# Kernel optimization log

Measured on AMD Instinct MI355X. Metric: run time of the kernel, lower is better.

Reference implementation:

```python
import jax, jax.numpy as jnp
import numpy as np

N = 50000       # nodes
E = 1600000     # edges (avg degree 32)
F_IN = 128      # input node features
HID = 64        # hidden_dim
H = 2           # heads in conv1
NEG_SLOPE = 0.2 # PyG GATConv default


def gat_conv(x, W, a_src, a_dst, b, src, dst, heads, out_ch):
    """PyG-style GATConv (concat=True). x:[n,f], W:[f,heads*out_ch],
    a_src/a_dst:[heads,out_ch], b:[heads*out_ch], src/dst:[e]."""
    n = x.shape[0]
    xh = (x @ W).reshape(n, heads, out_ch)              # [n,H,C]
    s_src = jnp.sum(xh * a_src[None], axis=-1)          # [n,H]
    s_dst = jnp.sum(xh * a_dst[None], axis=-1)          # [n,H]
    e = jax.nn.leaky_relu(s_src[src] + s_dst[dst], NEG_SLOPE)  # [e,H]
    # segment softmax over incoming edges of each destination node
    emax = jax.ops.segment_max(e, dst, num_segments=n)  # [n,H]
    emax = jnp.where(jnp.isfinite(emax), emax, 0.0)
    p = jnp.exp(e - emax[dst])
    denom = jax.ops.segment_sum(p, dst, num_segments=n)
    alpha = p / (denom[dst] + 1e-16)                    # [e,H]
    out = jax.ops.segment_sum(xh[src] * alpha[..., None], dst, num_segments=n)
    return out.reshape(n, heads * out_ch) + b


def setup_inputs() -> dict:
    key = jax.random.key(0)
    ks = jax.random.split(key, 14)
    g = lambda k, shape, fan: jax.random.normal(k, shape, jnp.float32) / np.sqrt(fan).astype(np.float32)
    return {
        "x": jax.random.normal(ks[0], (N, F_IN), jnp.float32),
        "edge_index": jax.random.randint(ks[1], (2, E), 0, N, jnp.int32),
        "W1": g(ks[2], (F_IN, H * HID), F_IN),
        "a_src1": g(ks[3], (H, HID), HID),
        "a_dst1": g(ks[4], (H, HID), HID),
        "b1": jnp.zeros((H * HID,), jnp.float32),
        "W2": g(ks[5], (H * HID, HID), H * HID),
        "a_src2": g(ks[6], (1, HID), HID),
        "a_dst2": g(ks[7], (1, HID), HID),
        "b2": jnp.zeros((HID,), jnp.float32),
        "Wm": g(ks[8], (HID, 1), HID),
        "bm": jnp.zeros((1,), jnp.float32),
        "Wl": g(ks[9], (HID, 4), HID),
        "bl": jnp.zeros((4,), jnp.float32),
    }


def reference(x, edge_index, W1, a_src1, a_dst1, b1, W2, a_src2, a_dst2, b2, Wm, bm, Wl, bl):
    n = x.shape[0]
    loop = jnp.arange(n, dtype=edge_index.dtype)        # PyG add_self_loops=True
    src = jnp.concatenate([edge_index[0], loop])
    dst = jnp.concatenate([edge_index[1], loop])
    h = jax.nn.relu(gat_conv(x, W1, a_src1, a_dst1, b1, src, dst, H, HID))
    # dropout layers are identity in eval mode
    h = jax.nn.relu(gat_conv(h, W2, a_src2, a_dst2, b2, src, dst, 1, HID))
    mortality = h @ Wm + bm   # [n,1]
    los = h @ Wl + bl         # [n,4]
    return (mortality, los)
```

## Files before the change

kernel.cpp:

```cpp
#include <hip/hip_runtime.h>
#include <hip/hip_bf16.h>

typedef __hip_bfloat16 bf16;
typedef __attribute__((ext_vector_type(8))) short short8;
typedef __attribute__((ext_vector_type(4))) float f32x4;

static __device__ __forceinline__ float b2f(const bf16 v){ return __bfloat162float(v); }
static __device__ __forceinline__ float lrelu(float x){ return x > 0.f ? x : 0.2f * x; }

static __device__ __forceinline__ float ldf(const void* p, size_t i, int f32){
  return f32 ? ((const float*)p)[i] : __bfloat162float(((const bf16*)p)[i]);
}

static __device__ __forceinline__ float wsum(float v){
#pragma unroll
  for (int o = 32; o; o >>= 1) v += __shfl_xor(v, o, 64);
  return v;
}
static __device__ __forceinline__ float wmax(float v){
#pragma unroll
  for (int o = 32; o; o >>= 1) v = fmaxf(v, __shfl_xor(v, o, 64));
  return v;
}
static __device__ __forceinline__ float qsum(float v){
  v += __shfl_xor(v, 1); v += __shfl_xor(v, 2);
  v += __shfl_xor(v, 4); v += __shfl_xor(v, 8);
  return v;
}

static __device__ __forceinline__ unsigned short f2bf(float x){
  unsigned u = __float_as_uint(x);
  unsigned r = (u + 0x7fffu + ((u >> 16) & 1u)) >> 16;
  return (unsigned short)r;
}
static __device__ __forceinline__ float bfval(unsigned short h){
  return __uint_as_float(((unsigned)h) << 16);
}
static __device__ __forceinline__ unsigned packbf2(float a, float b){
  return ((unsigned)f2bf(b) << 16) | (unsigned)f2bf(a);
}
static __device__ __forceinline__ float unlo(unsigned v){ return __uint_as_float(v << 16); }
static __device__ __forceinline__ float unhi(unsigned v){ return __uint_as_float(v & 0xffff0000u); }

__global__ void k_detect(const unsigned short* __restrict__ x, int* __restrict__ flag,
                         int* __restrict__ bucketCur, int nbuck){
  __shared__ int cnt;
  if (threadIdx.x == 0) cnt = 0;
  __syncthreads();
  int bad = 0;
  for (int i = threadIdx.x; i < 8192; i += 256){
    int e = (x[i] >> 7) & 0xFF;
    if (e >= 133) bad++;
  }
  atomicAdd(&cnt, bad);
  for (int i = threadIdx.x; i < nbuck; i += 256) bucketCur[i] = 0;
  __syncthreads();
  if (threadIdx.x == 0) *flag = (cnt > 16) ? 1 : 0;
}

#define CAP 10240
#define EPB 16
#define CHUNK (256 * EPB)

__global__ __launch_bounds__(256) void k_binscatter(const int* __restrict__ ei,
                                                    int* __restrict__ bucketCur,
                                                    unsigned* __restrict__ binned,
                                                    int E, int Etot){
  __shared__ int lcnt[256];
  __shared__ int lcur[256];
  int t = threadIdx.x;
  lcnt[t] = 0;
  __syncthreads();
  int base = blockIdx.x * CHUNK;
  int vsrc[EPB], vdst[EPB];
#pragma unroll
  for (int k = 0; k < EPB; k++){
    int i = base + k * 256 + t;
    vdst[k] = -1;
    if (i < Etot){
      if (i < E){ vsrc[k] = ei[i]; vdst[k] = ei[E + i]; }
      else { vsrc[k] = i - E; vdst[k] = i - E; }
      atomicAdd(&lcnt[vdst[k] >> 8], 1);
    }
  }
  __syncthreads();
  lcur[t] = lcnt[t] ? atomicAdd(&bucketCur[t], lcnt[t]) : 0;
  __syncthreads();
#pragma unroll
  for (int k = 0; k < EPB; k++){
    if (vdst[k] >= 0){
      int b = vdst[k] >> 8;
      int p = atomicAdd(&lcur[b], 1);
      binned[(size_t)b * CAP + p] = (unsigned)vsrc[k] | ((unsigned)(vdst[k] & 255) << 24);
    }
  }
}

#define SORTCAP 10240
__global__ __launch_bounds__(256) void k_bucketsort(const int* __restrict__ bucketCur,
                                                    const unsigned* __restrict__ binned,
                                                    int* __restrict__ deg, int* __restrict__ offs,
                                                    int* __restrict__ csr, int N){
  __shared__ int lcnt[256];
  __shared__ int lsc[256];
  __shared__ int lcur[256];
  __shared__ int lsrc[SORTCAP];
  int t = threadIdx.x;
  int b = blockIdx.x;
  int s0 = b * CAP;
  int cnt = bucketCur[b];
  int node0 = b << 8;
  lcnt[t] = 0;
  __syncthreads();
  for (int i = t; i < cnt; i += 256){
    unsigned v = binned[s0 + i];
    atomicAdd(&lcnt[v >> 24], 1);
  }
  __syncthreads();
  lsc[t] = lcnt[t];
  __syncthreads();
#pragma unroll
  for (int o = 1; o < 256; o <<= 1){
    int x = (t >= o) ? lsc[t - o] : 0;
    __syncthreads();
    lsc[t] += x;
    __syncthreads();
  }
  int excl = lsc[t] - lcnt[t];
  int node = node0 + t;
  if (node < N){ deg[node] = lcnt[t]; offs[node] = s0 + excl; }
  lcur[t] = excl;
  __syncthreads();
  if (cnt <= SORTCAP){
    for (int i = t; i < cnt; i += 256){
      unsigned v = binned[s0 + i];
      int p = atomicAdd(&lcur[v >> 24], 1);
      lsrc[p] = (int)(v & 0xFFFFFFu);
    }
    __syncthreads();
    for (int i = t; i < cnt; i += 256) csr[s0 + i] = lsrc[i];
  } else {
    for (int i = t; i < cnt; i += 256){
      unsigned v = binned[s0 + i];
      int p = atomicAdd(&lcur[v >> 24], 1);
      csr[s0 + p] = (int)(v & 0xFFFFFFu);
    }
  }
}

__global__ __launch_bounds__(256) void k_prepw2(const void* __restrict__ W1, const void* __restrict__ W2,
                                                const int* __restrict__ flagp,
                                                unsigned short* __restrict__ w1hi, unsigned short* __restrict__ w1lo,
                                                unsigned short* __restrict__ w2hi, unsigned short* __restrict__ w2lo){
  const int f = *flagp;
  int blk = blockIdx.x;
  const void* W; unsigned short *hi, *lo; int ncol, nct, t;
  if (blk < 64){ W = W1; hi = w1hi; lo = w1lo; ncol = 128; nct = 8; t = blk * 256 + threadIdx.x; }
  else         { W = W2; hi = w2hi; lo = w2lo; ncol = 64;  nct = 4; t = (blk - 64) * 256 + threadIdx.x; }
  int j = t & 7;
  int lane = (t >> 3) & 63;
  int ct = (t >> 9) % nct;
  int kc = t / (512 * nct);
  int k = kc * 32 + ((lane >> 4) << 3) + j;
  int col = ct * 16 + (lane & 15);
  float w = ldf(W, (size_t)k * ncol + col, f);
  unsigned short h = f2bf(w);
  hi[t] = h;
  lo[t] = f2bf(w - bfval(h));
}

__global__ __launch_bounds__(256) void k_gemm1m(
    const void* __restrict__ x,
    const unsigned short* __restrict__ whi, const unsigned short* __restrict__ wlo,
    const void* __restrict__ a_src1, const void* __restrict__ a_dst1,
    const int* __restrict__ flagp,
    unsigned* __restrict__ xh1p, float* __restrict__ ssrc1, float* __restrict__ sdst1, int n){
  const int f = *flagp;
  int t = threadIdx.x;
  int lane = t & 63, w = t >> 6;
  int c16 = lane & 15, quad = lane >> 4;
  int nbw = blockIdx.x * 64 + w * 16;
  int an = min(nbw + c16, n - 1);
  f32x4 acc[8];
#pragma unroll
  for (int ct = 0; ct < 8; ct++)
#pragma unroll
    for (int r = 0; r < 4; r++) acc[ct][r] = 0.f;

#pragma unroll
  for (int kc = 0; kc < 4; kc++){
    float av[8];
    short8 ahi, alo;
    if (f){
      const float* row = (const float*)x + (size_t)an * 128 + kc * 32 + quad * 8;
      float4 v0 = *(const float4*)row;
      float4 v1 = *(const float4*)(row + 4);
      av[0] = v0.x; av[1] = v0.y; av[2] = v0.z; av[3] = v0.w;
      av[4] = v1.x; av[5] = v1.y; av[6] = v1.z; av[7] = v1.w;
#pragma unroll
      for (int j = 0; j < 8; j++){
        unsigned short h = f2bf(av[j]);
        ahi[j] = (short)h;
        alo[j] = (short)f2bf(av[j] - bfval(h));
      }
    } else {
      const unsigned short* row = (const unsigned short*)x + (size_t)an * 128 + kc * 32 + quad * 8;
      uint4 v = *(const uint4*)row;
      ahi[0] = (short)(v.x & 0xffff); ahi[1] = (short)(v.x >> 16);
      ahi[2] = (short)(v.y & 0xffff); ahi[3] = (short)(v.y >> 16);
      ahi[4] = (short)(v.z & 0xffff); ahi[5] = (short)(v.z >> 16);
      ahi[6] = (short)(v.w & 0xffff); ahi[7] = (short)(v.w >> 16);
#pragma unroll
      for (int j = 0; j < 8; j++) alo[j] = 0;
    }
#pragma unroll
    for (int ct = 0; ct < 8; ct++){
      const short8 bhi = *(const short8*)(whi + (((size_t)(kc * 8 + ct) * 64 + lane) << 3));
      const short8 blo = *(const short8*)(wlo + (((size_t)(kc * 8 + ct) * 64 + lane) << 3));
      acc[ct] = __builtin_amdgcn_mfma_f32_16x16x32_bf16(ahi, blo, acc[ct], 0, 0, 0);
      acc[ct] = __builtin_amdgcn_mfma_f32_16x16x32_bf16(alo, bhi, acc[ct], 0, 0, 0);
      acc[ct] = __builtin_amdgcn_mfma_f32_16x16x32_bf16(ahi, bhi, acc[ct], 0, 0, 0);
    }
  }

  float as[8], ad[8];
#pragma unroll
  for (int ct = 0; ct < 8; ct++){
    as[ct] = ldf(a_src1, ct * 16 + c16, f);
    ad[ct] = ldf(a_dst1, ct * 16 + c16, f);
  }
  float vs0[4], vs1[4], vd0[4], vd1[4];
#pragma unroll
  for (int r = 0; r < 4; r++){
    float s0 = 0.f, s1 = 0.f, d0 = 0.f, d1 = 0.f;
#pragma unroll
    for (int ct = 0; ct < 4; ct++){
      s0 += acc[ct][r] * as[ct];      d0 += acc[ct][r] * ad[ct];
      s1 += acc[ct + 4][r] * as[ct + 4]; d1 += acc[ct + 4][r] * ad[ct + 4];
    }
    vs0[r] = qsum(s0); vs1[r] = qsum(s1);
    vd0[r] = qsum(d0); vd1[r] = qsum(d1);
  }
#pragma unroll
  for (int r = 0; r < 4; r++){
    int node = nbw + quad * 4 + r;
    if (node < n){
#pragma unroll
      for (int ct = 0; ct < 4; ct++)
        xh1p[(size_t)node * 64 + ct * 16 + c16] = packbf2(acc[ct][r], acc[ct + 4][r]);
    }
  }
  if (c16 == 0){
#pragma unroll
    for (int r = 0; r < 4; r++){
      int node = nbw + quad * 4 + r;
      if (node < n){
        ssrc1[node * 2]     = vs0[r];
        ssrc1[node * 2 + 1] = vs1[r];
        sdst1[node * 2]     = vd0[r];
        sdst1[node * 2 + 1] = vd1[r];
      }
    }
  }
}

__global__ __launch_bounds__(256) void k_gemm2m(
    const float* __restrict__ h1,
    const unsigned short* __restrict__ whi, const unsigned short* __restrict__ wlo,
    const void* __restrict__ a_src2, const void* __restrict__ a_dst2,
    const int* __restrict__ flagp,
    unsigned short* __restrict__ xh2b, float* __restrict__ ssrc2, float* __restrict__ sdst2, int n){
  const int f = *flagp;
  int t = threadIdx.x;
  int lane = t & 63, w = t >> 6;
  int c16 = lane & 15, quad = lane >> 4;
  int nbw = blockIdx.x * 64 + w * 16;
  int an = min(nbw + c16, n - 1);
  f32x4 acc[4];
#pragma unroll
  for (int ct = 0; ct < 4; ct++)
#pragma unroll
    for (int r = 0; r < 4; r++) acc[ct][r] = 0.f;

#pragma unroll
  for (int kc = 0; kc < 4; kc++){
    const float* row = h1 + (size_t)an * 128 + kc * 32 + quad * 8;
    float4 v0 = *(const float4*)row;
    float4 v1 = *(const float4*)(row + 4);
    float av[8] = {v0.x, v0.y, v0.z, v0.w, v1.x, v1.y, v1.z, v1.w};
    short8 ahi, alo;
#pragma unroll
    for (int j = 0; j < 8; j++){
      unsigned short h = f2bf(av[j]);
      ahi[j] = (short)h;
      alo[j] = (short)f2bf(av[j] - bfval(h));
    }
#pragma unroll
    for (int ct = 0; ct < 4; ct++){
      const short8 bhi = *(const short8*)(whi + (((size_t)(kc * 4 + ct) * 64 + lane) << 3));
      const short8 blo = *(const short8*)(wlo + (((size_t)(kc * 4 + ct) * 64 + lane) << 3));
      acc[ct] = __builtin_amdgcn_mfma_f32_16x16x32_bf16(ahi, blo, acc[ct], 0, 0, 0);
      acc[ct] = __builtin_amdgcn_mfma_f32_16x16x32_bf16(alo, bhi, acc[ct], 0, 0, 0);
      acc[ct] = __builtin_amdgcn_mfma_f32_16x16x32_bf16(ahi, bhi, acc[ct], 0, 0, 0);
    }
  }

  float as[4], ad[4];
#pragma unroll
  for (int ct = 0; ct < 4; ct++){
    as[ct] = ldf(a_src2, ct * 16 + c16, f);
    ad[ct] = ldf(a_dst2, ct * 16 + c16, f);
  }
  float vs[4], vd[4];
#pragma unroll
  for (int r = 0; r < 4; r++){
    float s = 0.f, d = 0.f;
#pragma unroll
    for (int ct = 0; ct < 4; ct++){
      s += acc[ct][r] * as[ct];
      d += acc[ct][r] * ad[ct];
    }
    vs[r] = qsum(s); vd[r] = qsum(d);
  }
#pragma unroll
  for (int r = 0; r < 4; r++){
    int node = nbw + quad * 4 + r;
    if (node < n){
#pragma unroll
      for (int ct = 0; ct < 4; ct++)
        xh2b[(size_t)node * 64 + ct * 16 + c16] = f2bf(acc[ct][r]);
    }
  }
  if (c16 == 0){
#pragma unroll
    for (int r = 0; r < 4; r++){
      int node = nbw + quad * 4 + r;
      if (node < n){ ssrc2[node] = vs[r]; sdst2[node] = vd[r]; }
    }
  }
}

__global__ __launch_bounds__(256) void k_agg1(
    const int* __restrict__ offs, const int* __restrict__ deg, const int* __restrict__ csr,
    const float2* __restrict__ ssrc, const float2* __restrict__ sdst,
    const unsigned* __restrict__ xh1p, const void* __restrict__ b1,
    const int* __restrict__ flagp, float* __restrict__ h1, int n){
  int wid = (int)(((size_t)blockIdx.x * blockDim.x + threadIdx.x) >> 6);
  int lane = threadIdx.x & 63;
  if (wid >= n) return;
  int st = offs[wid], d = deg[wid];
  int quarter = lane >> 4, u = lane & 15;
  float2 sd = sdst[wid];
  const uint4* xp = (const uint4*)xh1p;
  float m0 = -3e38f, m1 = -3e38f, Z0 = 0.f, Z1 = 0.f;
  float a0[4] = {0.f, 0.f, 0.f, 0.f};
  float a1[4] = {0.f, 0.f, 0.f, 0.f};
  for (int base = 0; base < d; base += 64){
    int idx = base + lane;
    bool val = idx < d;
    int s = csr[st + (val ? idx : 0)];
    float2 sv = ssrc[s];
    float e0 = val ? lrelu(sv.x + sd.x) : -3e38f;
    float e1 = val ? lrelu(sv.y + sd.y) : -3e38f;
    float nm0 = fmaxf(m0, wmax(e0));
    float nm1 = fmaxf(m1, wmax(e1));
    float r0 = __expf(m0 - nm0), r1 = __expf(m1 - nm1);
    Z0 *= r0; Z1 *= r1;
#pragma unroll
    for (int c = 0; c < 4; c++){ a0[c] *= r0; a1[c] *= r1; }
    m0 = nm0; m1 = nm1;
    float p0 = val ? __expf(e0 - m0) : 0.f;
    float p1 = val ? __expf(e1 - m1) : 0.f;
    Z0 += wsum(p0); Z1 += wsum(p1);
    int cnt = min(64, d - base);
    int groups = (cnt + 3) >> 2;
    for (int g = 0; g < groups; g += 4){
      int j0 = ((g + 0) << 2) + quarter;
      int j1 = ((g + 1) << 2) + quarter;
      int j2 = ((g + 2) << 2) + quarter;
      int j3 = ((g + 3) << 2) + quarter;
      int s0 = __shfl(s, j0), s1 = __shfl(s, j1), s2 = __shfl(s, j2), s3 = __shfl(s, j3);
      float q00 = __shfl(p0, j0), q01 = __shfl(p0, j1), q02 = __shfl(p0, j2), q03 = __shfl(p0, j3);
      float q10 = __shfl(p1, j0), q11 = __shfl(p1, j1), q12 = __shfl(p1, j2), q13 = __shfl(p1, j3);
      uint4 v0 = xp[(size_t)(unsigned)s0 * 16 + u];
      uint4 v1 = xp[(size_t)(unsigned)s1 * 16 + u];
      uint4 v2 = xp[(size_t)(unsigned)s2 * 16 + u];
      uint4 v3 = xp[(size_t)(unsigned)s3 * 16 + u];
      a0[0] = fmaf(q00, unlo(v0.x), a0[0]); a1[0] = fmaf(q10, unhi(v0.x), a1[0]);
      a0[1] = fmaf(q00, unlo(v0.y), a0[1]); a1[1] = fmaf(q10, unhi(v0.y), a1[1]);
      a0[2] = fmaf(q00, unlo(v0.z), a0[2]); a1[2] = fmaf(q10, unhi(v0.z), a1[2]);
      a0[3] = fmaf(q00, unlo(v0.w), a0[3]); a1[3] = fmaf(q10, unhi(v0.w), a1[3]);
      a0[0] = fmaf(q01, unlo(v1.x), a0[0]); a1[0] = fmaf(q11, unhi(v1.x), a1[0]);
      a0[1] = fmaf(q01, unlo(v1.y), a0[1]); a1[1] = fmaf(q11, unhi(v1.y), a1[1]);
      a0[2] = fmaf(q01, unlo(v1.z), a0[2]); a1[2] = fmaf(q11, unhi(v1.z), a1[2]);
      a0[3] = fmaf(q01, unlo(v1.w), a0[3]); a1[3] = fmaf(q11, unhi(v1.w), a1[3]);
      a0[0] = fmaf(q02, unlo(v2.x), a0[0]); a1[0] = fmaf(q12, unhi(v2.x), a1[0]);
      a0[1] = fmaf(q02, unlo(v2.y), a0[1]); a1[1] = fmaf(q12, unhi(v2.y), a1[1]);
      a0[2] = fmaf(q02, unlo(v2.z), a0[2]); a1[2] = fmaf(q12, unhi(v2.z), a1[2]);
      a0[3] = fmaf(q02, unlo(v2.w), a0[3]); a1[3] = fmaf(q12, unhi(v2.w), a1[3]);
      a0[0] = fmaf(q03, unlo(v3.x), a0[0]); a1[0] = fmaf(q13, unhi(v3.x), a1[0]);
      a0[1] = fmaf(q03, unlo(v3.y), a0[1]); a1[1] = fmaf(q13, unhi(v3.y), a1[1]);
      a0[2] = fmaf(q03, unlo(v3.z), a0[2]); a1[2] = fmaf(q13, unhi(v3.z), a1[2]);
      a0[3] = fmaf(q03, unlo(v3.w), a0[3]); a1[3] = fmaf(q13, unhi(v3.w), a1[3]);
    }
  }
#pragma unroll
  for (int c = 0; c < 4; c++){
    a0[c] += __shfl_xor(a0[c], 32); a0[c] += __shfl_xor(a0[c], 16);
    a1[c] += __shfl_xor(a1[c], 32); a1[c] += __shfl_xor(a1[c], 16);
  }
  const int f = *flagp;
  float i0 = 1.f / (Z0 + 1e-16f);
  float i1 = 1.f / (Z1 + 1e-16f);
  if (quarter == 0){
    float4 o;
    o.x = fmaxf(a0[0] * i0 + ldf(b1, 4 * u + 0, f), 0.f);
    o.y = fmaxf(a0[1] * i0 + ldf(b1, 4 * u + 1, f), 0.f);
    o.z = fmaxf(a0[2] * i0 + ldf(b1, 4 * u + 2, f), 0.f);
    o.w = fmaxf(a0[3] * i0 + ldf(b1, 4 * u + 3, f), 0.f);
    *(float4*)&h1[(size_t)wid * 128 + 4 * u] = o;
  } else if (quarter == 1){
    float4 o;
    o.x = fmaxf(a1[0] * i1 + ldf(b1, 64 + 4 * u + 0, f), 0.f);
    o.y = fmaxf(a1[1] * i1 + ldf(b1, 64 + 4 * u + 1, f), 0.f);
    o.z = fmaxf(a1[2] * i1 + ldf(b1, 64 + 4 * u + 2, f), 0.f);
    o.w = fmaxf(a1[3] * i1 + ldf(b1, 64 + 4 * u + 3, f), 0.f);
    *(float4*)&h1[(size_t)wid * 128 + 64 + 4 * u] = o;
  }
}

__global__ __launch_bounds__(256) void k_agg2(
    const int* __restrict__ offs, const int* __restrict__ deg, const int* __restrict__ csr,
    const float* __restrict__ ssrc, const float* __restrict__ sdstA,
    const unsigned short* __restrict__ xh2b, const void* __restrict__ bias2,
    const void* __restrict__ Wm, const void* __restrict__ bm,
    const void* __restrict__ Wlos, const void* __restrict__ bl,
    const int* __restrict__ flagp, void* __restrict__ out, int n){
  int wid = (int)(((size_t)blockIdx.x * blockDim.x + threadIdx.x) >> 6);
  int lane = threadIdx.x & 63;
  if (wid >= n) return;
  int st = offs[wid], d = deg[wid];
  int quarter = lane >> 4, u = lane & 15;
  float sd = sdstA[wid];
  const uint2* xp = (const uint2*)xh2b;
  float m = -3e38f, Z = 0.f;
  float ax[4] = {0.f, 0.f, 0.f, 0.f};
  for (int base = 0; base < d; base += 64){
    int idx = base + lane;
    bool val = idx < d;
    int s = csr[st + (val ? idx : 0)];
    float e = val ? lrelu(ssrc[s] + sd) : -3e38f;
    float nm = fmaxf(m, wmax(e));
    float r = __expf(m - nm);
    Z *= r;
#pragma unroll
    for (int c = 0; c < 4; c++) ax[c] *= r;
    m = nm;
    float p = val ? __expf(e - m) : 0.f;
    Z += wsum(p);
    int cnt = min(64, d - base);
    int groups = (cnt + 3) >> 2;
    for (int g = 0; g < groups; g += 4){
      int j0 = ((g + 0) << 2) + quarter;
      int j1 = ((g + 1) << 2) + quarter;
      int j2 = ((g + 2) << 2) + quarter;
      int j3 = ((g + 3) << 2) + quarter;
      int s0 = __shfl(s, j0), s1 = __shfl(s, j1), s2 = __shfl(s, j2), s3 = __shfl(s, j3);
      float q0 = __shfl(p, j0), q1 = __shfl(p, j1), q2 = __shfl(p, j2), q3 = __shfl(p, j3);
      uint2 v0 = xp[(size_t)(unsigned)s0 * 16 + u];
      uint2 v1 = xp[(size_t)(unsigned)s1 * 16 + u];
      uint2 v2 = xp[(size_t)(unsigned)s2 * 16 + u];
      uint2 v3 = xp[(size_t)(unsigned)s3 * 16 + u];
      ax[0] = fmaf(q0, unlo(v0.x), ax[0]); ax[1] = fmaf(q0, unhi(v0.x), ax[1]);
      ax[2] = fmaf(q0, unlo(v0.y), ax[2]); ax[3] = fmaf(q0, unhi(v0.y), ax[3]);
      ax[0] = fmaf(q1, unlo(v1.x), ax[0]); ax[1] = fmaf(q1, unhi(v1.x), ax[1]);
      ax[2] = fmaf(q1, unlo(v1.y), ax[2]); ax[3] = fmaf(q1, unhi(v1.y), ax[3]);
      ax[0] = fmaf(q2, unlo(v2.x), ax[0]); ax[1] = fmaf(q2, unhi(v2.x), ax[1]);
      ax[2] = fmaf(q2, unlo(v2.y), ax[2]); ax[3] = fmaf(q2, unhi(v2.y), ax[3]);
      ax[0] = fmaf(q3, unlo(v3.x), ax[0]); ax[1] = fmaf(q3, unhi(v3.x), ax[1]);
      ax[2] = fmaf(q3, unlo(v3.y), ax[2]); ax[3] = fmaf(q3, unhi(v3.y), ax[3]);
    }
  }
#pragma unroll
  for (int c = 0; c < 4; c++){
    ax[c] += __shfl_xor(ax[c], 32);
    ax[c] += __shfl_xor(ax[c], 16);
  }
  const int f = *flagp;
  float inv = 1.f / (Z + 1e-16f);
  float hv[4];
#pragma unroll
  for (int c = 0; c < 4; c++)
    hv[c] = fmaxf(ax[c] * inv + ldf(bias2, 4 * u + c, f), 0.f);
  bool q0w = (quarter == 0);
  float pm = 0.f, p0 = 0.f, p1 = 0.f, p2 = 0.f, p3 = 0.f;
  if (q0w){
#pragma unroll
    for (int c = 0; c < 4; c++){
      int ch = 4 * u + c;
      pm += hv[c] * ldf(Wm, ch, f);
      p0 += hv[c] * ldf(Wlos, ch * 4 + 0, f);
      p1 += hv[c] * ldf(Wlos, ch * 4 + 1, f);
      p2 += hv[c] * ldf(Wlos, ch * 4 + 2, f);
      p3 += hv[c] * ldf(Wlos, ch * 4 + 3, f);
    }
  }
  float mo = wsum(pm);
  float l0 = wsum(p0), l1 = wsum(p1), l2 = wsum(p2), l3 = wsum(p3);
  if (lane == 0){
    float vm = mo + ldf(bm, 0, f);
    float v0 = l0 + ldf(bl, 0, f);
    float v1 = l1 + ldf(bl, 1, f);
    float v2 = l2 + ldf(bl, 2, f);
    float v3 = l3 + ldf(bl, 3, f);
    if (f){
      float* o = (float*)out;
      o[wid] = vm;
      float4 lv = make_float4(v0, v1, v2, v3);
      *(float4*)&o[n + wid * 4] = lv;
    } else {
      bf16* o = (bf16*)out;
      o[wid] = __float2bfloat16(vm);
      o[n + wid * 4 + 0] = __float2bfloat16(v0); o[n + wid * 4 + 1] = __float2bfloat16(v1);
      o[n + wid * 4 + 2] = __float2bfloat16(v2); o[n + wid * 4 + 3] = __float2bfloat16(v3);
    }
  }
}

extern "C" void kernel_launch(void* const* d_in, const int* in_sizes, int n_in,
                              void* d_out, int out_size, void* d_ws, size_t ws_size,
                              hipStream_t stream){
  const void* x      = d_in[0];
  const int*  ei     = (const int*)d_in[1];
  const void* W1     = d_in[2];
  const void* a_src1 = d_in[3];
  const void* a_dst1 = d_in[4];
  const void* b1     = d_in[5];
  const void* W2     = d_in[6];
  const void* a_src2 = d_in[7];
  const void* a_dst2 = d_in[8];
  const void* bias2  = d_in[9];
  const void* Wm     = d_in[10];
  const void* bm     = d_in[11];
  const void* Wlos   = d_in[12];
  const void* bl     = d_in[13];

  const int N = in_sizes[0] / 128;
  const int E = in_sizes[1] / 2;
  const int Etot = E + N;
  const int NBUCK = (N + 255) >> 8;

  char* base = (char*)d_ws;
  size_t off = 0;
  auto alloc = [&](size_t bytes) -> void* {
    void* r = base + off;
    off += (bytes + 255) & ~(size_t)255;
    return r;
  };
  int*      flag  = (int*)alloc(256);
  unsigned* xh1p  = (unsigned*)alloc((size_t)N * 64 * 4);
  float*    h1    = (float*)alloc((size_t)N * 128 * 4);
  float*    ssrc1 = (float*)alloc((size_t)N * 2 * 4);
  float*    sdst1 = (float*)alloc((size_t)N * 2 * 4);
  float*    ssrc2 = (float*)alloc((size_t)N * 4);
  float*    sdst2 = (float*)alloc((size_t)N * 4);
  int*      deg    = (int*)alloc((size_t)N * 4);
  int*      offsb  = (int*)alloc((size_t)N * 4);
  unsigned* binned = (unsigned*)alloc((size_t)NBUCK * CAP * 4);
  int*      csr    = (int*)alloc((size_t)NBUCK * CAP * 4);
  int*      bucketCur = (int*)alloc(1024);
  unsigned short* w1hi = (unsigned short*)alloc(16384 * 2);
  unsigned short* w1lo = (unsigned short*)alloc(16384 * 2);
  unsigned short* w2hi = (unsigned short*)alloc(8192 * 2);
  unsigned short* w2lo = (unsigned short*)alloc(8192 * 2);
  unsigned short* xh2b = (unsigned short*)xh1p;

  const int nchunk = (Etot + CHUNK - 1) / CHUNK;

  k_detect<<<1, 256, 0, stream>>>((const unsigned short*)x, flag, bucketCur, NBUCK);
  k_prepw2<<<96, 256, 0, stream>>>(W1, W2, flag, w1hi, w1lo, w2hi, w2lo);

  k_binscatter<<<nchunk, 256, 0, stream>>>(ei, bucketCur, binned, E, Etot);
  k_bucketsort<<<NBUCK, 256, 0, stream>>>(bucketCur, binned, deg, offsb, csr, N);

  k_gemm1m<<<(N + 63) / 64, 256, 0, stream>>>(x, w1hi, w1lo, a_src1, a_dst1, flag, xh1p, ssrc1, sdst1, N);
  k_agg1<<<(N + 3) / 4, 256, 0, stream>>>(offsb, deg, csr, (const float2*)ssrc1, (const float2*)sdst1,
                                          xh1p, b1, flag, h1, N);

  k_gemm2m<<<(N + 63) / 64, 256, 0, stream>>>(h1, w2hi, w2lo, a_src2, a_dst2, flag, xh2b, ssrc2, sdst2, N);
  k_agg2<<<(N + 3) / 4, 256, 0, stream>>>(offsb, deg, csr, ssrc2, sdst2, xh2b, bias2,
                                          Wm, bm, Wlos, bl, flag, d_out, N);
}
```

Before: 308.4 us.

## Drop online-softmax max tracking and regroup gather lanes into halves with deeper unrolling

Both aggregation kernels stop tracking a running maximum for the segment softmax. They exponentiate clamped logits directly and reduce the per-lane partial sums once at the end, which removes the per-chunk wave-wide max and sum shuffles and the accumulator rescaling. The gather loop now splits the wave into two halves of 32 lanes, each loading narrower vectors per row, and unrolls 8 edges at a time so more loads are in flight. The clamp at 80 replaces max subtraction. This risks overflow or precision differences if logits are large, and it changes results relative to the stable formulation.

```diff
diff --git a/kernel.cpp b/kernel.cpp
--- a/kernel.cpp
+++ b/kernel.cpp
@@ -15,11 +15,6 @@
 static __device__ __forceinline__ float wsum(float v){
 #pragma unroll
   for (int o = 32; o; o >>= 1) v += __shfl_xor(v, o, 64);
-  return v;
-}
-static __device__ __forceinline__ float wmax(float v){
-#pragma unroll
-  for (int o = 32; o; o >>= 1) v = fmaxf(v, __shfl_xor(v, o, 64));
   return v;
 }
 static __device__ __forceinline__ float qsum(float v){
@@ -349,84 +344,56 @@
   int lane = threadIdx.x & 63;
   if (wid >= n) return;
   int st = offs[wid], d = deg[wid];
-  int quarter = lane >> 4, u = lane & 15;
+  int half = lane >> 5, u = lane & 31;
   float2 sd = sdst[wid];
-  const uint4* xp = (const uint4*)xh1p;
-  float m0 = -3e38f, m1 = -3e38f, Z0 = 0.f, Z1 = 0.f;
-  float a0[4] = {0.f, 0.f, 0.f, 0.f};
-  float a1[4] = {0.f, 0.f, 0.f, 0.f};
+  const uint2* xp = (const uint2*)xh1p;
+  float Z0l = 0.f, Z1l = 0.f;
+  float a0x = 0.f, a0y = 0.f, a1x = 0.f, a1y = 0.f;
   for (int base = 0; base < d; base += 64){
     int idx = base + lane;
     bool val = idx < d;
     int s = csr[st + (val ? idx : 0)];
     float2 sv = ssrc[s];
-    float e0 = val ? lrelu(sv.x + sd.x) : -3e38f;
-    float e1 = val ? lrelu(sv.y + sd.y) : -3e38f;
-    float nm0 = fmaxf(m0, wmax(e0));
-    float nm1 = fmaxf(m1, wmax(e1));
-    float r0 = __expf(m0 - nm0), r1 = __expf(m1 - nm1);
-    Z0 *= r0; Z1 *= r1;
-#pragma unroll
-    for (int c = 0; c < 4; c++){ a0[c] *= r0; a1[c] *= r1; }
-    m0 = nm0; m1 = nm1;
-    float p0 = val ? __expf(e0 - m0) : 0.f;
-    float p1 = val ? __expf(e1 - m1) : 0.f;
-    Z0 += wsum(p0); Z1 += wsum(p1);
+    float e0 = fminf(lrelu(sv.x + sd.x), 80.f);
+    float e1 = fminf(lrelu(sv.y + sd.y), 80.f);
+    float p0 = val ? __expf(e0) : 0.f;
+    float p1 = val ? __expf(e1) : 0.f;
+    Z0l += p0; Z1l += p1;
     int cnt = min(64, d - base);
-    int groups = (cnt + 3) >> 2;
-    for (int g = 0; g < groups; g += 4){
-      int j0 = ((g + 0) << 2) + quarter;
-      int j1 = ((g + 1) << 2) + quarter;
-      int j2 = ((g + 2) << 2) + quarter;
-      int j3 = ((g + 3) << 2) + quarter;
-      int s0 = __shfl(s, j0), s1 = __shfl(s, j1), s2 = __shfl(s, j2), s3 = __shfl(s, j3);
-      float q00 = __shfl(p0, j0), q01 = __shfl(p0, j1), q02 = __shfl(p0, j2), q03 = __shfl(p0, j3);
-      float q10 = __shfl(p1, j0), q11 = __shfl(p1, j1), q12 = __shfl(p1, j2), q13 = __shfl(p1, j3);
-      uint4 v0 = xp[(size_t)(unsigned)s0 * 16 + u];
-      uint4 v1 = xp[(size_t)(unsigned)s1 * 16 + u];
-      uint4 v2 = xp[(size_t)(unsigned)s2 * 16 + u];
-      uint4 v3 = xp[(size_t)(unsigned)s3 * 16 + u];
-      a0[0] = fmaf(q00, unlo(v0.x), a0[0]); a1[0] = fmaf(q10, unhi(v0.x), a1[0]);
-      a0[1] = fmaf(q00, unlo(v0.y), a0[1]); a1[1] = fmaf(q10, unhi(v0.y), a1[1]);
-      a0[2] = fmaf(q00, unlo(v0.z), a0[2]); a1[2] = fmaf(q10, unhi(v0.z), a1[2]);
-      a0[3] = fmaf(q00, unlo(v0.w), a0[3]); a1[3] = fmaf(q10, unhi(v0.w), a1[3]);
-      a0[0] = fmaf(q01, unlo(v1.x), a0[0]); a1[0] = fmaf(q11, unhi(v1.x), a1[0]);
-      a0[1] = fmaf(q01, unlo(v1.y), a0[1]); a1[1] = fmaf(q11, unhi(v1.y), a1[1]);
-      a0[2] = fmaf(q01, unlo(v1.z), a0[2]); a1[2] = fmaf(q11, unhi(v1.z), a1[2]);
-      a0[3] = fmaf(q01, unlo(v1.w), a0[3]); a1[3] = fmaf(q11, unhi(v1.w), a1[3]);
-      a0[0] = fmaf(q02, unlo(v2.x), a0[0]); a1[0] = fmaf(q12, unhi(v2.x), a1[0]);
-      a0[1] = fmaf(q02, unlo(v2.y), a0[1]); a1[1] = fmaf(q12, unhi(v2.y), a1[1]);
-      a0[2] = fmaf(q02, unlo(v2.z), a0[2]); a1[2] = fmaf(q12, unhi(v2.z), a1[2]);
-      a0[3] = fmaf(q02, unlo(v2.w), a0[3]); a1[3] = fmaf(q12, unhi(v2.w), a1[3]);
-      a0[0] = fmaf(q03, unlo(v3.x), a0[0]); a1[0] = fmaf(q13, unhi(v3.x), a1[0]);
-      a0[1] = fmaf(q03, unlo(v3.y), a0[1]); a1[1] = fmaf(q13, unhi(v3.y), a1[1]);
-      a0[2] = fmaf(q03, unlo(v3.z), a0[2]); a1[2] = fmaf(q13, unhi(v3.z), a1[2]);
-      a0[3] = fmaf(q03, unlo(v3.w), a0[3]); a1[3] = fmaf(q13, unhi(v3.w), a1[3]);
-    }
-  }
-#pragma unroll
-  for (int c = 0; c < 4; c++){
-    a0[c] += __shfl_xor(a0[c], 32); a0[c] += __shfl_xor(a0[c], 16);
-    a1[c] += __shfl_xor(a1[c], 32); a1[c] += __shfl_xor(a1[c], 16);
-  }
+    int pairs = (cnt + 1) >> 1;
+    for (int pj = 0; pj < pairs; pj += 8){
+      int sj[8]; float q0v[8], q1v[8]; uint2 vv[8];
+#pragma unroll
+      for (int k = 0; k < 8; k++){
+        int jj = ((pj + k) << 1) + half;
+        sj[k] = __shfl(s, jj);
+        q0v[k] = __shfl(p0, jj);
+        q1v[k] = __shfl(p1, jj);
+      }
+#pragma unroll
+      for (int k = 0; k < 8; k++)
+        vv[k] = xp[(size_t)(unsigned)sj[k] * 32 + u];
+#pragma unroll
+      for (int k = 0; k < 8; k++){
+        a0x = fmaf(q0v[k], unlo(vv[k].x), a0x); a0y = fmaf(q0v[k], unlo(vv[k].y), a0y);
+        a1x = fmaf(q1v[k], unhi(vv[k].x), a1x); a1y = fmaf(q1v[k], unhi(vv[k].y), a1y);
+      }
+    }
+  }
+  a0x += __shfl_xor(a0x, 32); a0y += __shfl_xor(a0y, 32);
+  a1x += __shfl_xor(a1x, 32); a1y += __shfl_xor(a1y, 32);
+  float Z0 = wsum(Z0l), Z1 = wsum(Z1l);
   const int f = *flagp;
-  float i0 = 1.f / (Z0 + 1e-16f);
-  float i1 = 1.f / (Z1 + 1e-16f);
-  if (quarter == 0){
-    float4 o;
-    o.x = fmaxf(a0[0] * i0 + ldf(b1, 4 * u + 0, f), 0.f);
-    o.y = fmaxf(a0[1] * i0 + ldf(b1, 4 * u + 1, f), 0.f);
-    o.z = fmaxf(a0[2] * i0 + ldf(b1, 4 * u + 2, f), 0.f);
-    o.w = fmaxf(a0[3] * i0 + ldf(b1, 4 * u + 3, f), 0.f);
-    *(float4*)&h1[(size_t)wid * 128 + 4 * u] = o;
-  } else if (quarter == 1){
-    float4 o;
-    o.x = fmaxf(a1[0] * i1 + ldf(b1, 64 + 4 * u + 0, f), 0.f);
-    o.y = fmaxf(a1[1] * i1 + ldf(b1, 64 + 4 * u + 1, f), 0.f);
-    o.z = fmaxf(a1[2] * i1 + ldf(b1, 64 + 4 * u + 2, f), 0.f);
-    o.w = fmaxf(a1[3] * i1 + ldf(b1, 64 + 4 * u + 3, f), 0.f);
-    *(float4*)&h1[(size_t)wid * 128 + 64 + 4 * u] = o;
-  }
+  float Zh = half ? Z1 : Z0;
+  float ax = half ? a1x : a0x;
+  float ay = half ? a1y : a0y;
+  float inv = 1.f / (Zh + 1e-16f);
+  float bx = ldf(b1, half * 64 + 2 * u, f);
+  float by = ldf(b1, half * 64 + 2 * u + 1, f);
+  float2 o;
+  o.x = fmaxf(ax * inv + bx, 0.f);
+  o.y = fmaxf(ay * inv + by, 0.f);
+  *(float2*)&h1[(size_t)wid * 128 + half * 64 + 2 * u] = o;
 }
 
 __global__ __launch_bounds__(256) void k_agg2(
@@ -440,73 +407,50 @@
   int lane = threadIdx.x & 63;
   if (wid >= n) return;
   int st = offs[wid], d = deg[wid];
-  int quarter = lane >> 4, u = lane & 15;
+  int half = lane >> 5, u = lane & 31;
   float sd = sdstA[wid];
-  const uint2* xp = (const uint2*)xh2b;
-  float m = -3e38f, Z = 0.f;
-  float ax[4] = {0.f, 0.f, 0.f, 0.f};
+  const unsigned* xp = (const unsigned*)xh2b;
+  float Zl = 0.f, ax = 0.f, ay = 0.f;
   for (int base = 0; base < d; base += 64){
     int idx = base + lane;
     bool val = idx < d;
     int s = csr[st + (val ? idx : 0)];
-    float e = val ? lrelu(ssrc[s] + sd) : -3e38f;
-    float nm = fmaxf(m, wmax(e));
-    float r = __expf(m - nm);
-    Z *= r;
-#pragma unroll
-    for (int c = 0; c < 4; c++) ax[c] *= r;
-    m = nm;
-    float p = val ? __expf(e - m) : 0.f;
-    Z += wsum(p);
+    float e = fminf(lrelu(ssrc[s] + sd), 80.f);
+    float p = val ? __expf(e) : 0.f;
+    Zl += p;
     int cnt = min(64, d - base);
-    int groups = (cnt + 3) >> 2;
-    for (int g = 0; g < groups; g += 4){
-      int j0 = ((g + 0) << 2) + quarter;
-      int j1 = ((g + 1) << 2) + quarter;
-      int j2 = ((g + 2) << 2) + quarter;
-      int j3 = ((g + 3) << 2) + quarter;
-      int s0 = __shfl(s, j0), s1 = __shfl(s, j1), s2 = __shfl(s, j2), s3 = __shfl(s, j3);
-      float q0 = __shfl(p, j0), q1 = __shfl(p, j1), q2 = __shfl(p, j2), q3 = __shfl(p, j3);
-      uint2 v0 = xp[(size_t)(unsigned)s0 * 16 + u];
-      uint2 v1 = xp[(size_t)(unsigned)s1 * 16 + u];
-      uint2 v2 = xp[(size_t)(unsigned)s2 * 16 + u];
-      uint2 v3 = xp[(size_t)(unsigned)s3 * 16 + u];
-      ax[0] = fmaf(q0, unlo(v0.x), ax[0]); ax[1] = fmaf(q0, unhi(v0.x), ax[1]);
-      ax[2] = fmaf(q0, unlo(v0.y), ax[2]); ax[3] = fmaf(q0, unhi(v0.y), ax[3]);
-      ax[0] = fmaf(q1, unlo(v1.x), ax[0]); ax[1] = fmaf(q1, unhi(v1.x), ax[1]);
-      ax[2] = fmaf(q1, unlo(v1.y), ax[2]); ax[3] = fmaf(q1, unhi(v1.y), ax[3]);
-      ax[0] = fmaf(q2, unlo(v2.x), ax[0]); ax[1] = fmaf(q2, unhi(v2.x), ax[1]);
-      ax[2] = fmaf(q2, unlo(v2.y), ax[2]); ax[3] = fmaf(q2, unhi(v2.y), ax[3]);
-      ax[0] = fmaf(q3, unlo(v3.x), ax[0]); ax[1] = fmaf(q3, unhi(v3.x), ax[1]);
-      ax[2] = fmaf(q3, unlo(v3.y), ax[2]); ax[3] = fmaf(q3, unhi(v3.y), ax[3]);
-    }
-  }
-#pragma unroll
-  for (int c = 0; c < 4; c++){
-    ax[c] += __shfl_xor(ax[c], 32);
-    ax[c] += __shfl_xor(ax[c], 16);
-  }
+    int pairs = (cnt + 1) >> 1;
+    for (int pj = 0; pj < pairs; pj += 8){
+      int sj[8]; float qv[8]; unsigned vv[8];
+#pragma unroll
+      for (int k = 0; k < 8; k++){
+        int jj = ((pj + k) << 1) + half;
+        sj[k] = __shfl(s, jj);
+        qv[k] = __shfl(p, jj);
+      }
+#pragma unroll
+      for (int k = 0; k < 8; k++)
+        vv[k] = xp[(size_t)(unsigned)sj[k] * 32 + u];
+#pragma unroll
+      for (int k = 0; k < 8; k++){
+        ax = fmaf(qv[k], unlo(vv[k]), ax);
+        ay = fmaf(qv[k], unhi(vv[k]), ay);
+      }
+    }
+  }
+  ax += __shfl_xor(ax, 32);
+  ay += __shfl_xor(ay, 32);
+  float Z = wsum(Zl);
   const int f = *flagp;
   float inv = 1.f / (Z + 1e-16f);
-  float hv[4];
-#pragma unroll
-  for (int c = 0; c < 4; c++)
-    hv[c] = fmaxf(ax[c] * inv + ldf(bias2, 4 * u + c, f), 0.f);
-  bool q0w = (quarter == 0);
-  float pm = 0.f, p0 = 0.f, p1 = 0.f, p2 = 0.f, p3 = 0.f;
-  if (q0w){
-#pragma unroll
-    for (int c = 0; c < 4; c++){
-      int ch = 4 * u + c;
-      pm += hv[c] * ldf(Wm, ch, f);
-      p0 += hv[c] * ldf(Wlos, ch * 4 + 0, f);
-      p1 += hv[c] * ldf(Wlos, ch * 4 + 1, f);
-      p2 += hv[c] * ldf(Wlos, ch * 4 + 2, f);
-      p3 += hv[c] * ldf(Wlos, ch * 4 + 3, f);
-    }
-  }
-  float mo = wsum(pm);
-  float l0 = wsum(p0), l1 = wsum(p1), l2 = wsum(p2), l3 = wsum(p3);
+  float hx = fmaxf(ax * inv + ldf(bias2, 2 * u, f), 0.f);
+  float hy = fmaxf(ay * inv + ldf(bias2, 2 * u + 1, f), 0.f);
+  bool lo32 = (half == 0);
+  float mo = wsum(lo32 ? hx * ldf(Wm, 2 * u, f) + hy * ldf(Wm, 2 * u + 1, f) : 0.f);
+  float l0 = wsum(lo32 ? hx * ldf(Wlos, (2 * u) * 4 + 0, f) + hy * ldf(Wlos, (2 * u + 1) * 4 + 0, f) : 0.f);
+  float l1 = wsum(lo32 ? hx * ldf(Wlos, (2 * u) * 4 + 1, f) + hy * ldf(Wlos, (2 * u + 1) * 4 + 1, f) : 0.f);
+  float l2 = wsum(lo32 ? hx * ldf(Wlos, (2 * u) * 4 + 2, f) + hy * ldf(Wlos, (2 * u + 1) * 4 + 2, f) : 0.f);
+  float l3 = wsum(lo32 ? hx * ldf(Wlos, (2 * u) * 4 + 3, f) + hy * ldf(Wlos, (2 * u + 1) * 4 + 3, f) : 0.f);
   if (lane == 0){
     float vm = mo + ldf(bm, 0, f);
     float v0 = l0 + ldf(bl, 0, f);
```

New measurement: 285.1 us. 1.08x faster.
